# Kernel optimization log

Hardware: AMD Instinct MI355X
Metric: run time of the kernel (lower is better)

The kernel has to match this reference:

```python
import jax, jax.numpy as jnp
import numpy as np

B, D, K, H, W = 2, 512, 32, 64, 64


def setup_inputs() -> dict:
    key = jax.random.key(0)
    k1, k2, k3 = jax.random.split(key, 3)
    X = jax.random.normal(k1, (B, D, H, W), dtype=jnp.float32)
    std1 = 1.0 / (K * D) ** 0.5
    codewords = jax.random.uniform(k2, (K, D), minval=-std1, maxval=std1, dtype=jnp.float32)
    scale = jax.random.uniform(k3, (D, K), minval=-1.0, maxval=0.0, dtype=jnp.float32)
    return {"X": X, "codewords": codewords, "scale": scale}


def reference(X, codewords, scale):
    # X: [B, D, H, W] -> x: [B, N, D], N = H*W
    Bv, Dv = X.shape[0], X.shape[1]
    x = X.reshape(Bv, Dv, -1).transpose(0, 2, 1)            # [B, N, D]
    # broadcast residual: x[b,n,d] - codewords[k,d], scaled per (d,k)
    residual = (x[:, :, :, None] - codewords.T) * scale     # [B, N, D, K]
    # soft assignment over K codewords
    Q = jax.nn.softmax(-0.5 * jnp.sum(residual * residual, axis=2), axis=2)  # [B, N, K]
    # weighted aggregation over N, normalized by per-codeword mass
    Z_num = jnp.einsum('bnk,bndk->bdk', Q, residual)        # [B, D, K]
    Z_ = Z_num / Q.sum(axis=1)[:, None, :]                  # [B, D, K]
    # L2-normalize along D
    Z = Z_ / jnp.sqrt(jnp.sum(Z_ * Z_, axis=1, keepdims=True))
    return (Z, Q)
```

## Files before the change

### kernel.cpp

```cpp
#include <hip/hip_runtime.h>
#include <math.h>

#define B_DIM 2
#define D_DIM 512
#define K_DIM 32
#define N_DIM 4096

__global__ __launch_bounds__(256, 2)
void k_dist_q(const float* __restrict__ X, const float* __restrict__ CW,
              const float* __restrict__ SC, float* __restrict__ Qout,
              float* __restrict__ nsq)
{
    __shared__ __align__(16) float xlds[16 * 516];
    __shared__ __align__(16) float red[16 * 16 * 36];

    const int tid = threadIdx.x;
    const int b  = blockIdx.x >> 8;
    const int n0 = (blockIdx.x & 255) << 4;
    const int dp = tid & 63;
    const int kp = tid >> 6;
    const int k0 = kp << 3;

    if (blockIdx.x == 0 && tid < 2 * K_DIM) nsq[tid] = 0.f;

    const float* xsrc = X + (size_t)b * D_DIM * N_DIM + n0;
#pragma unroll
    for (int j = 0; j < 8; ++j) {
        const int d  = (tid >> 2) + (j << 6);
        const int n4 = (tid & 3) << 2;
        float4 v = *(const float4*)(xsrc + (size_t)d * N_DIM + n4);
        xlds[(n4 + 0) * 516 + d] = v.x;
        xlds[(n4 + 1) * 516 + d] = v.y;
        xlds[(n4 + 2) * 516 + d] = v.z;
        xlds[(n4 + 3) * 516 + d] = v.w;
    }

    float cv[8][8];
#pragma unroll
    for (int kk = 0; kk < 8; ++kk) {
        const float* cr = CW + (k0 + kk) * D_DIM + (dp << 2);
        float4 c0 = *(const float4*)(cr);
        float4 c1 = *(const float4*)(cr + 256);
        cv[kk][0] = c0.x; cv[kk][1] = c0.y; cv[kk][2] = c0.z; cv[kk][3] = c0.w;
        cv[kk][4] = c1.x; cv[kk][5] = c1.y; cv[kk][6] = c1.z; cv[kk][7] = c1.w;
    }
    float Areg[8][8], Breg[8][8], ckp[8];
#pragma unroll
    for (int kk = 0; kk < 8; ++kk) ckp[kk] = 0.f;
#pragma unroll
    for (int dd = 0; dd < 8; ++dd) {
        const int d = (dd < 4) ? ((dp << 2) + dd) : (256 + (dp << 2) + (dd - 4));
        float4 s0 = *(const float4*)(SC + d * K_DIM + k0);
        float4 s1 = *(const float4*)(SC + d * K_DIM + k0 + 4);
        float sv[8] = {s0.x, s0.y, s0.z, s0.w, s1.x, s1.y, s1.z, s1.w};
#pragma unroll
        for (int kk = 0; kk < 8; ++kk) {
            float c = cv[kk][dd];
            float a = sv[kk] * sv[kk];
            Areg[dd][kk] = a;
            Breg[dd][kk] = -2.f * a * c;
            ckp[kk] = fmaf(a * c, c, ckp[kk]);
        }
    }
    __syncthreads();

#pragma unroll
    for (int n = 0; n < 16; ++n) {
        float dist[8];
#pragma unroll
        for (int kk = 0; kk < 8; ++kk) dist[kk] = ckp[kk];
        float4 xa = *(const float4*)(&xlds[n * 516 + (dp << 2)]);
        float4 xb = *(const float4*)(&xlds[n * 516 + (dp << 2) + 256]);
        float xv[8] = {xa.x, xa.y, xa.z, xa.w, xb.x, xb.y, xb.z, xb.w};
#pragma unroll
        for (int dd = 0; dd < 8; ++dd) {
            const float x  = xv[dd];
            const float x2 = x * x;
#pragma unroll
            for (int kk = 0; kk < 8; ++kk) {
                dist[kk] = fmaf(Areg[dd][kk], x2, dist[kk]);
                dist[kk] = fmaf(Breg[dd][kk], x,  dist[kk]);
            }
        }
#pragma unroll
        for (int kk = 0; kk < 8; ++kk) {
            dist[kk] += __shfl_xor(dist[kk], 32);
            dist[kk] += __shfl_xor(dist[kk], 16);
        }
        if (dp < 16) {
            float* r = &red[(n * 16 + dp) * 36 + k0];
            *(float4*)(r)     = make_float4(dist[0], dist[1], dist[2], dist[3]);
            *(float4*)(r + 4) = make_float4(dist[4], dist[5], dist[6], dist[7]);
        }
    }
    __syncthreads();

#pragma unroll
    for (int h = 0; h < 2; ++h) {
        const int n = (tid >> 5) + (h << 3);
        const int k = tid & 31;
        float dsum = 0.f;
#pragma unroll
        for (int i = 0; i < 16; ++i) dsum += red[(n * 16 + i) * 36 + k];
        float m = dsum;
#pragma unroll
        for (int mk = 16; mk >= 1; mk >>= 1)
            m = fminf(m, __shfl_xor(m, mk));
        float e = __expf(-0.5f * (dsum - m));
        float ssum = e;
#pragma unroll
        for (int mk = 16; mk >= 1; mk >>= 1)
            ssum += __shfl_xor(ssum, mk);
        Qout[((size_t)b * N_DIM + n0 + n) * K_DIM + k] = __fdividef(e, ssum);
    }
}

__global__ __launch_bounds__(256, 2)
void k_tpart(const float* __restrict__ X, const float* __restrict__ Qin,
             float* __restrict__ TP, float* __restrict__ Mpart)
{
    __shared__ __align__(16) float Xs[64 * 68];
    __shared__ __align__(16) float Qs[32 * 68];
    __shared__ __align__(16) float red4[4 * 64 * 36];
    __shared__ float mred[8][33];

    const int tid = threadIdx.x;
    const int bid = blockIdx.x;
    const int ns = bid & 31;
    const int dt = (bid >> 5) & 7;
    const int b  = bid >> 8;
    const int nsub = tid >> 5;
    const int dp = tid & 7;
    const int kp = (tid >> 3) & 3;
    const int wv = tid >> 6;

    float acc[8][8];
#pragma unroll
    for (int i = 0; i < 8; ++i)
#pragma unroll
        for (int j = 0; j < 8; ++j) acc[i][j] = 0.f;

    const float* xsrc = X + ((size_t)b * D_DIM + dt * 64) * N_DIM + ns * 128;
    const float* qsrc = Qin + ((size_t)b * N_DIM + ns * 128) * K_DIM;

    for (int ch = 0; ch < 2; ++ch) {
        __syncthreads();
#pragma unroll
        for (int i = 0; i < 4; ++i) {
            int flat4 = tid + (i << 8);
            int row = flat4 >> 4;
            int c4  = (flat4 & 15) << 2;
            float4 v = *(const float4*)(xsrc + (size_t)row * N_DIM + (ch << 6) + c4);
            *(float4*)(&Xs[row * 68 + c4]) = v;
        }
#pragma unroll
        for (int i = 0; i < 2; ++i) {
            int flat4 = tid + (i << 8);
            int nn = flat4 >> 3;
            int k4 = (flat4 & 7) << 2;
            float4 v = *(const float4*)(qsrc + ((ch << 6) + nn) * K_DIM + k4);
            Qs[(k4 + 0) * 68 + nn] = v.x;
            Qs[(k4 + 1) * 68 + nn] = v.y;
            Qs[(k4 + 2) * 68 + nn] = v.z;
            Qs[(k4 + 3) * 68 + nn] = v.w;
        }
        __syncthreads();
#pragma unroll
        for (int s = 0; s < 2; ++s) {
            const int nb = (nsub << 3) + (s << 2);
            float4 xr[8], qr[8];
#pragma unroll
            for (int i = 0; i < 8; ++i)
                xr[i] = *(const float4*)(&Xs[(dp + (i << 3)) * 68 + nb]);
#pragma unroll
            for (int j = 0; j < 8; ++j)
                qr[j] = *(const float4*)(&Qs[(kp + (j << 2)) * 68 + nb]);
#pragma unroll
            for (int i = 0; i < 8; ++i)
#pragma unroll
                for (int j = 0; j < 8; ++j) {
                    acc[i][j] = fmaf(xr[i].x, qr[j].x, acc[i][j]);
                    acc[i][j] = fmaf(xr[i].y, qr[j].y, acc[i][j]);
                    acc[i][j] = fmaf(xr[i].z, qr[j].z, acc[i][j]);
                    acc[i][j] = fmaf(xr[i].w, qr[j].w, acc[i][j]);
                }
        }
    }
    __syncthreads();
#pragma unroll
    for (int i = 0; i < 8; ++i)
#pragma unroll
        for (int j = 0; j < 8; ++j)
            acc[i][j] += __shfl_xor(acc[i][j], 32);
    if ((tid & 32) == 0) {
#pragma unroll
        for (int i = 0; i < 8; ++i)
#pragma unroll
            for (int j = 0; j < 8; ++j)
                red4[(wv * 64 + dp + (i << 3)) * 36 + kp + (j << 2)] = acc[i][j];
    }
    __syncthreads();
    float* dst = TP + (((size_t)ns * 2 + b) * D_DIM + dt * 64) * K_DIM;
#pragma unroll
    for (int e = 0; e < 8; ++e) {
        int flat = tid + (e << 8);
        int dl = flat >> 5;
        int k  = flat & 31;
        float s = red4[(0 * 64 + dl) * 36 + k] + red4[(1 * 64 + dl) * 36 + k]
                + red4[(2 * 64 + dl) * 36 + k] + red4[(3 * 64 + dl) * 36 + k];
        dst[dl * K_DIM + k] = s;
    }
    if (dt == 0) {
        const int k = tid & 31, g = tid >> 5;
        float qm = 0.f;
#pragma unroll
        for (int n = 0; n < 16; ++n)
            qm += qsrc[(g * 16 + n) * K_DIM + k];
        mred[g][k] = qm;
        __syncthreads();
        if (tid < K_DIM) {
            float t = 0.f;
#pragma unroll
            for (int i = 0; i < 8; ++i) t += mred[i][tid];
            Mpart[(ns * B_DIM + b) * K_DIM + tid] = t;
        }
    }
}

__global__ __launch_bounds__(256)
void k_zpre(const float* __restrict__ TP, const float* __restrict__ Mpart,
            const float* __restrict__ CW, const float* __restrict__ SC,
            float* __restrict__ Ztmp, float* __restrict__ nsq)
{
    __shared__ float part[8][33];
    const int tid = threadIdx.x;
    const int b  = blockIdx.x >> 6;
    const int ds = blockIdx.x & 63;
    const int d  = (ds << 3) + (tid >> 5);
    const int k  = tid & 31;
    float sum = 0.f;
#pragma unroll
    for (int ns = 0; ns < 32; ++ns)
        sum += TP[(((size_t)ns * 2 + b) * D_DIM + d) * K_DIM + k];
    float m = 0.f;
#pragma unroll
    for (int ns = 0; ns < 32; ++ns)
        m += Mpart[(ns * B_DIM + b) * K_DIM + k];
    float c = CW[k * D_DIM + d];
    float s = SC[d * K_DIM + k];
    float z = s * (sum / m - c);
    Ztmp[((size_t)b * D_DIM + d) * K_DIM + k] = z;
    part[tid >> 5][k] = z * z;
    __syncthreads();
    if (tid < K_DIM) {
        float t = 0.f;
#pragma unroll
        for (int i = 0; i < 8; ++i) t += part[i][tid];
        atomicAdd(&nsq[b * K_DIM + tid], t);
    }
}

__global__ __launch_bounds__(256)
void k_zfin(const float* __restrict__ Ztmp, const float* __restrict__ nsq,
            float* __restrict__ Z)
{
    const int tid = threadIdx.x;
    const int b  = blockIdx.x >> 6;
    const int ds = blockIdx.x & 63;
    const int d  = (ds << 3) + (tid >> 5);
    const int k  = tid & 31;
    const int idx = ((b * D_DIM) + d) * K_DIM + k;
    Z[idx] = Ztmp[idx] * rsqrtf(nsq[b * K_DIM + k]);
}

extern "C" void kernel_launch(void* const* d_in, const int* in_sizes, int n_in,
                              void* d_out, int out_size, void* d_ws, size_t ws_size,
                              hipStream_t stream)
{
    const float* X  = (const float*)d_in[0];
    const float* CW = (const float*)d_in[1];
    const float* SC = (const float*)d_in[2];
    float* Z = (float*)d_out;
    float* Q = (float*)d_out + B_DIM * D_DIM * K_DIM;

    float* W    = (float*)d_ws;
    float* nsq  = W;
    float* Mpart= W + 64;
    float* TP   = W + 64 + 2048;
    float* ZT   = TP + 32 * B_DIM * D_DIM * K_DIM;

    k_dist_q<<<512, 256, 0, stream>>>(X, CW, SC, Q, nsq);
    k_tpart <<<512, 256, 0, stream>>>(X, Q, TP, Mpart);
    k_zpre  <<<128, 256, 0, stream>>>(TP, Mpart, CW, SC, ZT, nsq);
    k_zfin  <<<128, 256, 0, stream>>>(ZT, nsq, Z);
}
```

Before: 96.29 us.

## Use packed FP32 FMA in distance and aggregation kernels, fuse Z finalize

Rewrites the inner FMA loops of the distance/softmax kernel and the Q^T X aggregation kernel with inline v_pk_fma_f32, which handles two lanes of float math per instruction. The Q tile in shared memory is now stored row-major so it can be read as vectors. The two final Z kernels are merged into one that uses a global atomic counter as a grid barrier, so the normalization happens in place and the Ztmp round-trip and one launch go away. The spin barrier assumes all 128 blocks are resident at the same time, and the inline asm ties the code to CDNA packed-math encoding.

```diff
diff --git a/kernel.cpp b/kernel.cpp
--- a/kernel.cpp
+++ b/kernel.cpp
@@ -6,10 +6,21 @@
 #define K_DIM 32
 #define N_DIM 4096
 
+typedef float v2f __attribute__((ext_vector_type(2)));
+
+__device__ __forceinline__ void pk_bl(v2f& d, v2f a, v2f b) {
+    asm("v_pk_fma_f32 %0, %1, %2, %0 op_sel:[0,0,0] op_sel_hi:[1,0,1]"
+        : "+v"(d) : "v"(a), "v"(b));
+}
+__device__ __forceinline__ void pk_bh(v2f& d, v2f a, v2f b) {
+    asm("v_pk_fma_f32 %0, %1, %2, %0 op_sel:[0,1,0] op_sel_hi:[1,1,1]"
+        : "+v"(d) : "v"(a), "v"(b));
+}
+
 __global__ __launch_bounds__(256, 2)
 void k_dist_q(const float* __restrict__ X, const float* __restrict__ CW,
               const float* __restrict__ SC, float* __restrict__ Qout,
-              float* __restrict__ nsq)
+              float* __restrict__ nsq, int* __restrict__ cnt)
 {
     __shared__ __align__(16) float xlds[16 * 516];
     __shared__ __align__(16) float red[16 * 16 * 36];
@@ -21,7 +32,10 @@
     const int kp = tid >> 6;
     const int k0 = kp << 3;
 
-    if (blockIdx.x == 0 && tid < 2 * K_DIM) nsq[tid] = 0.f;
+    if (blockIdx.x == 0) {
+        if (tid < 64) nsq[tid] = 0.f;
+        if (tid == 64) *cnt = 0;
+    }
 
     const float* xsrc = X + (size_t)b * D_DIM * N_DIM + n0;
 #pragma unroll
@@ -44,9 +58,9 @@
         cv[kk][0] = c0.x; cv[kk][1] = c0.y; cv[kk][2] = c0.z; cv[kk][3] = c0.w;
         cv[kk][4] = c1.x; cv[kk][5] = c1.y; cv[kk][6] = c1.z; cv[kk][7] = c1.w;
     }
-    float Areg[8][8], Breg[8][8], ckp[8];
-#pragma unroll
-    for (int kk = 0; kk < 8; ++kk) ckp[kk] = 0.f;
+    v2f A2[8][4], B2r[8][4], ckp2[4];
+#pragma unroll
+    for (int kk2 = 0; kk2 < 4; ++kk2) ckp2[kk2] = (v2f)(0.f);
 #pragma unroll
     for (int dd = 0; dd < 8; ++dd) {
         const int d = (dd < 4) ? ((dp << 2) + dd) : (256 + (dp << 2) + (dd - 4));
@@ -54,34 +68,41 @@
         float4 s1 = *(const float4*)(SC + d * K_DIM + k0 + 4);
         float sv[8] = {s0.x, s0.y, s0.z, s0.w, s1.x, s1.y, s1.z, s1.w};
 #pragma unroll
-        for (int kk = 0; kk < 8; ++kk) {
-            float c = cv[kk][dd];
-            float a = sv[kk] * sv[kk];
-            Areg[dd][kk] = a;
-            Breg[dd][kk] = -2.f * a * c;
-            ckp[kk] = fmaf(a * c, c, ckp[kk]);
+        for (int kk2 = 0; kk2 < 4; ++kk2) {
+#pragma unroll
+            for (int h = 0; h < 2; ++h) {
+                const int kk = 2 * kk2 + h;
+                float c = cv[kk][dd];
+                float a = sv[kk] * sv[kk];
+                A2[dd][kk2][h]  = a;
+                B2r[dd][kk2][h] = -2.f * a * c;
+                ckp2[kk2][h] = fmaf(a * c, c, ckp2[kk2][h]);
+            }
         }
     }
     __syncthreads();
 
 #pragma unroll
     for (int n = 0; n < 16; ++n) {
-        float dist[8];
-#pragma unroll
-        for (int kk = 0; kk < 8; ++kk) dist[kk] = ckp[kk];
+        v2f d2[4];
+#pragma unroll
+        for (int kk2 = 0; kk2 < 4; ++kk2) d2[kk2] = ckp2[kk2];
         float4 xa = *(const float4*)(&xlds[n * 516 + (dp << 2)]);
         float4 xb = *(const float4*)(&xlds[n * 516 + (dp << 2) + 256]);
-        float xv[8] = {xa.x, xa.y, xa.z, xa.w, xb.x, xb.y, xb.z, xb.w};
-#pragma unroll
-        for (int dd = 0; dd < 8; ++dd) {
-            const float x  = xv[dd];
-            const float x2 = x * x;
-#pragma unroll
-            for (int kk = 0; kk < 8; ++kk) {
-                dist[kk] = fmaf(Areg[dd][kk], x2, dist[kk]);
-                dist[kk] = fmaf(Breg[dd][kk], x,  dist[kk]);
+        v2f xp[4] = {{xa.x, xa.y}, {xa.z, xa.w}, {xb.x, xb.y}, {xb.z, xb.w}};
+#pragma unroll
+        for (int dq = 0; dq < 4; ++dq) {
+            v2f x2p = xp[dq] * xp[dq];
+#pragma unroll
+            for (int kk2 = 0; kk2 < 4; ++kk2) {
+                pk_bl(d2[kk2], A2[2 * dq][kk2],      x2p);
+                pk_bl(d2[kk2], B2r[2 * dq][kk2],     xp[dq]);
+                pk_bh(d2[kk2], A2[2 * dq + 1][kk2],  x2p);
+                pk_bh(d2[kk2], B2r[2 * dq + 1][kk2], xp[dq]);
             }
         }
+        float dist[8] = {d2[0].x, d2[0].y, d2[1].x, d2[1].y,
+                         d2[2].x, d2[2].y, d2[3].x, d2[3].y};
 #pragma unroll
         for (int kk = 0; kk < 8; ++kk) {
             dist[kk] += __shfl_xor(dist[kk], 32);
@@ -120,7 +141,7 @@
              float* __restrict__ TP, float* __restrict__ Mpart)
 {
     __shared__ __align__(16) float Xs[64 * 68];
-    __shared__ __align__(16) float Qs[32 * 68];
+    __shared__ __align__(16) float Qs[64 * 36];
     __shared__ __align__(16) float red4[4 * 64 * 36];
     __shared__ float mred[8][33];
 
@@ -132,13 +153,14 @@
     const int nsub = tid >> 5;
     const int dp = tid & 7;
     const int kp = (tid >> 3) & 3;
+    const int k0t = kp << 3;
     const int wv = tid >> 6;
 
-    float acc[8][8];
+    v2f acc2[8][4];
 #pragma unroll
     for (int i = 0; i < 8; ++i)
 #pragma unroll
-        for (int j = 0; j < 8; ++j) acc[i][j] = 0.f;
+        for (int j = 0; j < 4; ++j) acc2[i][j] = (v2f)(0.f);
 
     const float* xsrc = X + ((size_t)b * D_DIM + dt * 64) * N_DIM + ns * 128;
     const float* qsrc = Qin + ((size_t)b * N_DIM + ns * 128) * K_DIM;
@@ -158,46 +180,55 @@
             int flat4 = tid + (i << 8);
             int nn = flat4 >> 3;
             int k4 = (flat4 & 7) << 2;
-            float4 v = *(const float4*)(qsrc + ((ch << 6) + nn) * K_DIM + k4);
-            Qs[(k4 + 0) * 68 + nn] = v.x;
-            Qs[(k4 + 1) * 68 + nn] = v.y;
-            Qs[(k4 + 2) * 68 + nn] = v.z;
-            Qs[(k4 + 3) * 68 + nn] = v.w;
+            *(float4*)(&Qs[nn * 36 + k4]) =
+                *(const float4*)(qsrc + ((ch << 6) + nn) * K_DIM + k4);
         }
         __syncthreads();
 #pragma unroll
         for (int s = 0; s < 2; ++s) {
             const int nb = (nsub << 3) + (s << 2);
-            float4 xr[8], qr[8];
+            float4 xr[8];
 #pragma unroll
             for (int i = 0; i < 8; ++i)
                 xr[i] = *(const float4*)(&Xs[(dp + (i << 3)) * 68 + nb]);
 #pragma unroll
-            for (int j = 0; j < 8; ++j)
-                qr[j] = *(const float4*)(&Qs[(kp + (j << 2)) * 68 + nb]);
-#pragma unroll
-            for (int i = 0; i < 8; ++i)
-#pragma unroll
-                for (int j = 0; j < 8; ++j) {
-                    acc[i][j] = fmaf(xr[i].x, qr[j].x, acc[i][j]);
-                    acc[i][j] = fmaf(xr[i].y, qr[j].y, acc[i][j]);
-                    acc[i][j] = fmaf(xr[i].z, qr[j].z, acc[i][j]);
-                    acc[i][j] = fmaf(xr[i].w, qr[j].w, acc[i][j]);
+            for (int n = 0; n < 4; ++n) {
+                float4 qa = *(const float4*)(&Qs[(nb + n) * 36 + k0t]);
+                float4 qb = *(const float4*)(&Qs[(nb + n) * 36 + k0t + 4]);
+                v2f q2[4] = {{qa.x, qa.y}, {qa.z, qa.w}, {qb.x, qb.y}, {qb.z, qb.w}};
+#pragma unroll
+                for (int i = 0; i < 8; ++i) {
+                    v2f xlo = {xr[i].x, xr[i].y};
+                    v2f xhi = {xr[i].z, xr[i].w};
+                    v2f xb2 = (n < 2) ? xlo : xhi;
+                    if ((n & 1) == 0) {
+#pragma unroll
+                        for (int j = 0; j < 4; ++j) pk_bl(acc2[i][j], q2[j], xb2);
+                    } else {
+#pragma unroll
+                        for (int j = 0; j < 4; ++j) pk_bh(acc2[i][j], q2[j], xb2);
+                    }
                 }
+            }
         }
     }
     __syncthreads();
 #pragma unroll
     for (int i = 0; i < 8; ++i)
 #pragma unroll
-        for (int j = 0; j < 8; ++j)
-            acc[i][j] += __shfl_xor(acc[i][j], 32);
+        for (int j = 0; j < 4; ++j) {
+            acc2[i][j].x += __shfl_xor(acc2[i][j].x, 32);
+            acc2[i][j].y += __shfl_xor(acc2[i][j].y, 32);
+        }
     if ((tid & 32) == 0) {
 #pragma unroll
-        for (int i = 0; i < 8; ++i)
-#pragma unroll
-            for (int j = 0; j < 8; ++j)
-                red4[(wv * 64 + dp + (i << 3)) * 36 + kp + (j << 2)] = acc[i][j];
+        for (int i = 0; i < 8; ++i) {
+            float* r = &red4[(wv * 64 + dp + (i << 3)) * 36 + k0t];
+            *(float4*)(r)     = make_float4(acc2[i][0].x, acc2[i][0].y,
+                                            acc2[i][1].x, acc2[i][1].y);
+            *(float4*)(r + 4) = make_float4(acc2[i][2].x, acc2[i][2].y,
+                                            acc2[i][3].x, acc2[i][3].y);
+        }
     }
     __syncthreads();
     float* dst = TP + (((size_t)ns * 2 + b) * D_DIM + dt * 64) * K_DIM;
@@ -228,9 +259,9 @@
 }
 
 __global__ __launch_bounds__(256)
-void k_zpre(const float* __restrict__ TP, const float* __restrict__ Mpart,
-            const float* __restrict__ CW, const float* __restrict__ SC,
-            float* __restrict__ Ztmp, float* __restrict__ nsq)
+void k_zfuse(const float* __restrict__ TP, const float* __restrict__ Mpart,
+             const float* __restrict__ CW, const float* __restrict__ SC,
+             float* __restrict__ Z, float* __restrict__ nsq, int* __restrict__ cnt)
 {
     __shared__ float part[8][33];
     const int tid = threadIdx.x;
@@ -249,7 +280,6 @@
     float c = CW[k * D_DIM + d];
     float s = SC[d * K_DIM + k];
     float z = s * (sum / m - c);
-    Ztmp[((size_t)b * D_DIM + d) * K_DIM + k] = z;
     part[tid >> 5][k] = z * z;
     __syncthreads();
     if (tid < K_DIM) {
@@ -258,19 +288,16 @@
         for (int i = 0; i < 8; ++i) t += part[i][tid];
         atomicAdd(&nsq[b * K_DIM + tid], t);
     }
-}
-
-__global__ __launch_bounds__(256)
-void k_zfin(const float* __restrict__ Ztmp, const float* __restrict__ nsq,
-            float* __restrict__ Z)
-{
-    const int tid = threadIdx.x;
-    const int b  = blockIdx.x >> 6;
-    const int ds = blockIdx.x & 63;
-    const int d  = (ds << 3) + (tid >> 5);
-    const int k  = tid & 31;
-    const int idx = ((b * D_DIM) + d) * K_DIM + k;
-    Z[idx] = Ztmp[idx] * rsqrtf(nsq[b * K_DIM + k]);
+    __syncthreads();
+    if (tid == 0) {
+        __hip_atomic_fetch_add(cnt, 1, __ATOMIC_ACQ_REL, __HIP_MEMORY_SCOPE_AGENT);
+        while (__hip_atomic_load(cnt, __ATOMIC_ACQUIRE, __HIP_MEMORY_SCOPE_AGENT) < 128)
+            __builtin_amdgcn_s_sleep(1);
+    }
+    __syncthreads();
+    float nv = __hip_atomic_load(&nsq[b * K_DIM + k], __ATOMIC_RELAXED,
+                                 __HIP_MEMORY_SCOPE_AGENT);
+    Z[((b * D_DIM) + d) * K_DIM + k] = z * rsqrtf(nv);
 }
 
 extern "C" void kernel_launch(void* const* d_in, const int* in_sizes, int n_in,
@@ -285,12 +312,11 @@
 
     float* W    = (float*)d_ws;
     float* nsq  = W;
-    float* Mpart= W + 64;
-    float* TP   = W + 64 + 2048;
-    float* ZT   = TP + 32 * B_DIM * D_DIM * K_DIM;
-
-    k_dist_q<<<512, 256, 0, stream>>>(X, CW, SC, Q, nsq);
+    int*   cnt  = (int*)(W + 64);
+    float* Mpart= W + 128;
+    float* TP   = W + 128 + 2048;
+
+    k_dist_q<<<512, 256, 0, stream>>>(X, CW, SC, Q, nsq, cnt);
     k_tpart <<<512, 256, 0, stream>>>(X, Q, TP, Mpart);
-    k_zpre  <<<128, 256, 0, stream>>>(TP, Mpart, CW, SC, ZT, nsq);
-    k_zfin  <<<128, 256, 0, stream>>>(ZT, nsq, Z);
-}
+    k_zfuse <<<128, 256, 0, stream>>>(TP, Mpart, CW, SC, Z, nsq, cnt);
+}
```

New measurement: 99.31 us. 1.03x slower.
